# Performance work log

Hardware: AMD Instinct MI355X
Metric: run time of the kernel (lower is better)

Reference implementation:

```python
import jax, jax.numpy as jnp
import numpy as np

EMB_DIM = 400
NUM_ENT = 100000
NUM_REL = 200
OUT_CH = 6
STRIDE = 2
MAX_ARITY = 3
ARITY = 3
BATCH = 8192
W_OUT = (EMB_DIM - 1) // STRIDE + 1          # conv output width (filt_w=1, stride=2)
FC_LEN = OUT_CH * W_OUT                      # 1200


def setup_inputs() -> dict:
    key = jax.random.key(0)
    ks = jax.random.split(key, 10)
    r_idx = jax.random.randint(ks[0], (BATCH,), 0, NUM_REL)
    E_mat = jax.random.randint(ks[1], (BATCH, ARITY), 0, NUM_ENT)
    ms = jax.random.normal(ks[2], (BATCH, ARITY), dtype=jnp.float32)
    bs = jax.random.normal(ks[3], (BATCH, ARITY), dtype=jnp.float32)
    E_emb = jax.random.normal(ks[4], (NUM_ENT, EMB_DIM), dtype=jnp.float32) * 0.05
    R_emb = jax.random.normal(ks[5], (NUM_REL, EMB_DIM), dtype=jnp.float32) * 0.05
    fc2_W = jax.random.normal(ks[6], (OUT_CH, MAX_ARITY + 1), dtype=jnp.float32) * 0.1
    fc2_b = jax.random.normal(ks[7], (OUT_CH,), dtype=jnp.float32) * 0.1
    fc_W = jax.random.normal(ks[8], (EMB_DIM, FC_LEN), dtype=jnp.float32) * 0.02
    fc_b = jax.random.normal(ks[9], (EMB_DIM,), dtype=jnp.float32) * 0.02
    return {"r_idx": r_idx, "E_mat": E_mat, "ms": ms, "bs": bs,
            "E_emb": E_emb, "R_emb": R_emb,
            "fc2_W": fc2_W, "fc2_b": fc2_b, "fc_W": fc_W, "fc_b": fc_b}


def _convolve(E_emb, fc2_W, fc2_b, fc_W, fc_b, e_idx, pos):
    # Embedding gather: (B, D)
    e = E_emb[e_idx]
    # 1x1 grouped conv with stride=2 == strided slice of the embedding: (B, W_OUT)
    e_s = e[:, ::STRIDE]
    # Hypernetwork filter from fc2(one_hot(pos)) -- identical across batch: (OUT_CH,)
    k = fc2_W[:, pos] + fc2_b
    # Per-sample outer product, flattened oc-major (matches torch view order): (B, FC_LEN)
    feat = (k[None, :, None] * e_s[:, None, :]).reshape(e.shape[0], FC_LEN)
    # fc: Linear(FC_LEN, EMB_DIM)
    return jnp.einsum('bf,df->bd', feat, fc_W) + fc_b


def reference(r_idx, E_mat, ms, bs, E_emb, R_emb, fc2_W, fc2_b, fc_W, fc_b):
    r = R_emb[r_idx]                                        # (B, D)
    x = None
    for i in range(E_mat.shape[1]):                         # small fixed arity loop
        e = _convolve(E_emb, fc2_W, fc2_b, fc_W, fc_b, E_mat[:, i], i)
        e = e * ms[:, i][:, None] + bs[:, i][:, None]
        x = e if x is None else x * e
    x = x * r
    return jnp.sum(x, axis=1)                               # (B,)
```

## Files before the change

### kernel.cpp

```cpp
#include <hip/hip_runtime.h>

typedef __attribute__((ext_vector_type(8))) short bf16x8;
typedef __attribute__((ext_vector_type(4))) float f32x4;

#define EMB_DIM 400
#define OUT_CH  6
#define ARITY   3
#define BATCH   8192
#define W_OUT   200
#define FC_LEN  1200
#define NT      25
#define NKS     7
#define BM      32
#define NTASK   (ARITY * BM * 100)
#define NLD     19

static __device__ __forceinline__ ushort f2bf(float f) {
    union { float f; uint u; } v; v.f = f;
    uint u = v.u;
    return (ushort)((u + 0x7FFF + ((u >> 16) & 1)) >> 16);
}

__global__ __launch_bounds__(256)
void pack_M(const float* __restrict__ fc2_W, const float* __restrict__ fc2_b,
            const float* __restrict__ fc_W, ushort* __restrict__ Mb) {
    __shared__ float Bt[32][16];
    const int bid = blockIdx.x;
    const int kk  = blockIdx.y;
    const int i = bid / NT, t = bid % NT;
    float kc[OUT_CH];
#pragma unroll
    for (int c = 0; c < OUT_CH; ++c) kc[c] = fc2_W[c * 4 + i] + fc2_b[c];
    const int tid = threadIdx.x;
    const int dd = tid >> 4, wl = tid & 15;
    const int d = t * 16 + dd;
#pragma unroll
    for (int s = 0; s < 2; ++s) {
        int w = kk * 32 + wl + 16 * s;
        float v = 0.f;
        if (w < W_OUT) {
#pragma unroll
            for (int c = 0; c < OUT_CH; ++c)
                v = fmaf(kc[c], fc_W[d * FC_LEN + c * W_OUT + w], v);
        }
        Bt[wl + 16 * s][dd] = v;
    }
    __syncthreads();
    if (tid < 64) {
        const int l = tid;
        ushort vals[8];
#pragma unroll
        for (int j = 0; j < 8; ++j)
            vals[j] = f2bf(Bt[(l >> 4) * 8 + j][l & 15]);
        *reinterpret_cast<uint4*>(Mb + ((size_t)(bid * NKS + kk) * 64 + l) * 8) =
            *reinterpret_cast<const uint4*>(vals);
    }
}

__global__ __launch_bounds__(512)
void hype_mfma(const int* __restrict__ r_idx, const int* __restrict__ E_mat,
               const float* __restrict__ ms, const float* __restrict__ bs,
               const float* __restrict__ E_emb, const float* __restrict__ R_emb,
               const float* __restrict__ fc_b, const ushort* __restrict__ Mb,
               float* __restrict__ out) {
    __shared__ ushort es[ARITY * 2 * NKS * 64 * 8];
    __shared__ float sm_ms[BM * 3], sm_bs[BM * 3], sm_fcb[EMB_DIM];
    __shared__ int   sm_rb[BM], sm_ent[BM * 3];
    __shared__ float osum[4][BM];

    const int tid = threadIdx.x;
    const int b0 = blockIdx.x * BM;

    if (tid < BM * 3) {
        sm_ms[tid]  = ms[b0 * 3 + tid];
        sm_bs[tid]  = bs[b0 * 3 + tid];
        sm_ent[tid] = E_mat[b0 * 3 + tid];
    }
    if (tid >= 96 && tid < 96 + BM) sm_rb[tid - 96] = r_idx[b0 + tid - 96] * EMB_DIM;
    for (int z = tid; z < EMB_DIM; z += 512) sm_fcb[z] = fc_b[z];

    uint* esu = reinterpret_cast<uint*>(es);
    for (int z = tid; z < ARITY * 2 * 192; z += 512) {
        int pair = z / 192, off = z % 192;
        esu[(pair * NKS + 6) * 256 + 64 + off] = 0;
    }
    __syncthreads();

    float4 vreg[NLD];
#pragma unroll
    for (int k = 0; k < NLD; ++k) {
        int tq = tid + k * 512;
        if (tq < NTASK) {
            int q = tq % 100;
            int p = tq / 100;
            int i = p / BM, r = p % BM;
            int ent = sm_ent[r * 3 + i];
            vreg[k] = *reinterpret_cast<const float4*>(
                E_emb + (size_t)ent * EMB_DIM + 4 * q);
        }
    }
#pragma unroll
    for (int k = 0; k < NLD; ++k) {
        int tq = tid + k * 512;
        if (tq < NTASK) {
            int q = tq % 100;
            int p = tq / 100;
            int i = p / BM, r = p % BM;
            int w = 2 * q;
            int kk = w >> 5;
            int lsub = (w >> 3) & 3;
            int j = w & 7;
            int rg = r >> 4, rl = r & 15;
            int l = lsub * 16 + rl;
            uint pk = (uint)f2bf(vreg[k].x) | ((uint)f2bf(vreg[k].z) << 16);
            esu[(((i * 2 + rg) * NKS + kk) * 64 + l) * 4 + (j >> 1)] = pk;
        }
    }
    __syncthreads();

    const int wid = tid >> 6;
    const int lane = tid & 63;
    const int rg = wid & 1, cg = wid >> 1;
    const int cl = lane & 15;
    const int rql = lane >> 4;

    bf16x8 afrag[ARITY][NKS];
#pragma unroll
    for (int i = 0; i < ARITY; ++i)
#pragma unroll
        for (int kk = 0; kk < NKS; ++kk)
            afrag[i][kk] = *reinterpret_cast<const bf16x8*>(
                es + (((i * 2 + rg) * NKS + kk) * 64 + lane) * 8);

    float msv[ARITY][4], bsv[ARITY][4];
    int rbv[4];
#pragma unroll
    for (int r_ = 0; r_ < 4; ++r_) {
        int row = rg * 16 + rql * 4 + r_;
#pragma unroll
        for (int i = 0; i < ARITY; ++i) {
            msv[i][r_] = sm_ms[row * 3 + i];
            bsv[i][r_] = sm_bs[row * 3 + i];
        }
        rbv[r_] = sm_rb[row];
    }

    float rowsum[4] = {0.f, 0.f, 0.f, 0.f};
    for (int t = cg; t < NT; t += 4) {
        f32x4 acc[ARITY];
#pragma unroll
        for (int i = 0; i < ARITY; ++i) {
            f32x4 a = {0.f, 0.f, 0.f, 0.f};
            const ushort* bp = Mb + ((size_t)(i * NT + t) * NKS * 64 + lane) * 8;
#pragma unroll
            for (int kk = 0; kk < NKS; ++kk) {
                bf16x8 bfr = *reinterpret_cast<const bf16x8*>(bp + kk * 512);
                a = __builtin_amdgcn_mfma_f32_16x16x32_bf16(afrag[i][kk], bfr, a, 0, 0, 0);
            }
            acc[i] = a;
        }
        const int d = t * 16 + cl;
        const float fcb = sm_fcb[d];
#pragma unroll
        for (int r_ = 0; r_ < 4; ++r_) {
            float Rr = R_emb[rbv[r_] + d];
            float e0 = fmaf(acc[0][r_] + fcb, msv[0][r_], bsv[0][r_]);
            float e1 = fmaf(acc[1][r_] + fcb, msv[1][r_], bsv[1][r_]);
            float e2 = fmaf(acc[2][r_] + fcb, msv[2][r_], bsv[2][r_]);
            rowsum[r_] = fmaf(e0 * e1 * e2, Rr, rowsum[r_]);
        }
    }

#pragma unroll
    for (int m = 1; m < 16; m <<= 1)
#pragma unroll
        for (int r_ = 0; r_ < 4; ++r_)
            rowsum[r_] += __shfl_xor(rowsum[r_], m, 64);
    if (cl == 0) {
#pragma unroll
        for (int r_ = 0; r_ < 4; ++r_)
            osum[cg][rg * 16 + rql * 4 + r_] = rowsum[r_];
    }
    __syncthreads();
    if (tid < BM)
        out[b0 + tid] = osum[0][tid] + osum[1][tid] + osum[2][tid] + osum[3][tid];
}

extern "C" void kernel_launch(void* const* d_in, const int* in_sizes, int n_in,
                              void* d_out, int out_size, void* d_ws, size_t ws_size,
                              hipStream_t stream) {
    const int*   r_idx = (const int*)d_in[0];
    const int*   E_mat = (const int*)d_in[1];
    const float* ms    = (const float*)d_in[2];
    const float* bs    = (const float*)d_in[3];
    const float* E_emb = (const float*)d_in[4];
    const float* R_emb = (const float*)d_in[5];
    const float* fc2_W = (const float*)d_in[6];
    const float* fc2_b = (const float*)d_in[7];
    const float* fc_W  = (const float*)d_in[8];
    const float* fc_b  = (const float*)d_in[9];
    float*  out = (float*)d_out;
    ushort* Mb  = (ushort*)d_ws;

    pack_M<<<dim3(ARITY * NT, NKS), 256, 0, stream>>>(fc2_W, fc2_b, fc_W, Mb);
    hype_mfma<<<BATCH / BM, 512, 0, stream>>>(r_idx, E_mat, ms, bs, E_emb, R_emb,
                                              fc_b, Mb, out);
}
```

Measured before the change: 34.08 us.

## Have each wave cover both row groups to reuse B fragments across MFMAs

Each wave now loads A fragments for both 16-row groups and computes both against the same B fragment, with column tiles split across 8 waves instead of 4. This halves global loads of the packed weight matrix per block and doubles MFMA work per B load. It raises register pressure, since the A fragments double, and gives coarser load balance over the 25 column tiles. The per-row scale, bias and index values are now read from shared memory inside the loop instead of being held in registers.

After: 44.77 us. +31.4%, slower.

```diff
diff --git a/kernel.cpp b/kernel.cpp
--- a/kernel.cpp
+++ b/kernel.cpp
@@ -66,7 +66,7 @@
     __shared__ ushort es[ARITY * 2 * NKS * 64 * 8];
     __shared__ float sm_ms[BM * 3], sm_bs[BM * 3], sm_fcb[EMB_DIM];
     __shared__ int   sm_rb[BM], sm_ent[BM * 3];
-    __shared__ float osum[4][BM];
+    __shared__ float osum[8][BM];
 
     const int tid = threadIdx.x;
     const int b0 = blockIdx.x * BM;
@@ -118,72 +118,76 @@
     }
     __syncthreads();
 
-    const int wid = tid >> 6;
+    const int wv   = tid >> 6;
     const int lane = tid & 63;
-    const int rg = wid & 1, cg = wid >> 1;
-    const int cl = lane & 15;
-    const int rql = lane >> 4;
-
-    bf16x8 afrag[ARITY][NKS];
-#pragma unroll
-    for (int i = 0; i < ARITY; ++i)
-#pragma unroll
-        for (int kk = 0; kk < NKS; ++kk)
-            afrag[i][kk] = *reinterpret_cast<const bf16x8*>(
-                es + (((i * 2 + rg) * NKS + kk) * 64 + lane) * 8);
-
-    float msv[ARITY][4], bsv[ARITY][4];
-    int rbv[4];
-#pragma unroll
-    for (int r_ = 0; r_ < 4; ++r_) {
-        int row = rg * 16 + rql * 4 + r_;
+    const int cl   = lane & 15;
+    const int rql  = lane >> 4;
+
+    bf16x8 afrag[2][ARITY][NKS];
+#pragma unroll
+    for (int rg = 0; rg < 2; ++rg)
+#pragma unroll
+        for (int i = 0; i < ARITY; ++i)
+#pragma unroll
+            for (int kk = 0; kk < NKS; ++kk)
+                afrag[rg][i][kk] = *reinterpret_cast<const bf16x8*>(
+                    es + (((i * 2 + rg) * NKS + kk) * 64 + lane) * 8);
+
+    float rowsum[2][4] = {{0.f, 0.f, 0.f, 0.f}, {0.f, 0.f, 0.f, 0.f}};
+    for (int t = wv; t < NT; t += 8) {
+        f32x4 acc[2][ARITY];
+#pragma unroll
+        for (int rg = 0; rg < 2; ++rg)
+#pragma unroll
+            for (int i = 0; i < ARITY; ++i) acc[rg][i] = (f32x4){0.f, 0.f, 0.f, 0.f};
 #pragma unroll
         for (int i = 0; i < ARITY; ++i) {
-            msv[i][r_] = sm_ms[row * 3 + i];
-            bsv[i][r_] = sm_bs[row * 3 + i];
-        }
-        rbv[r_] = sm_rb[row];
-    }
-
-    float rowsum[4] = {0.f, 0.f, 0.f, 0.f};
-    for (int t = cg; t < NT; t += 4) {
-        f32x4 acc[ARITY];
-#pragma unroll
-        for (int i = 0; i < ARITY; ++i) {
-            f32x4 a = {0.f, 0.f, 0.f, 0.f};
             const ushort* bp = Mb + ((size_t)(i * NT + t) * NKS * 64 + lane) * 8;
 #pragma unroll
             for (int kk = 0; kk < NKS; ++kk) {
                 bf16x8 bfr = *reinterpret_cast<const bf16x8*>(bp + kk * 512);
-                a = __builtin_amdgcn_mfma_f32_16x16x32_bf16(afrag[i][kk], bfr, a, 0, 0, 0);
+                acc[0][i] = __builtin_amdgcn_mfma_f32_16x16x32_bf16(
+                    afrag[0][i][kk], bfr, acc[0][i], 0, 0, 0);
+                acc[1][i] = __builtin_amdgcn_mfma_f32_16x16x32_bf16(
+                    afrag[1][i][kk], bfr, acc[1][i], 0, 0, 0);
             }
-            acc[i] = a;
         }
         const int d = t * 16 + cl;
         const float fcb = sm_fcb[d];
 #pragma unroll
-        for (int r_ = 0; r_ < 4; ++r_) {
-            float Rr = R_emb[rbv[r_] + d];
-            float e0 = fmaf(acc[0][r_] + fcb, msv[0][r_], bsv[0][r_]);
-            float e1 = fmaf(acc[1][r_] + fcb, msv[1][r_], bsv[1][r_]);
-            float e2 = fmaf(acc[2][r_] + fcb, msv[2][r_], bsv[2][r_]);
-            rowsum[r_] = fmaf(e0 * e1 * e2, Rr, rowsum[r_]);
-        }
+        for (int rg = 0; rg < 2; ++rg)
+#pragma unroll
+            for (int r_ = 0; r_ < 4; ++r_) {
+                int row = rg * 16 + rql * 4 + r_;
+                float Rr = R_emb[sm_rb[row] + d];
+                float e0 = fmaf(acc[rg][0][r_] + fcb, sm_ms[row * 3 + 0], sm_bs[row * 3 + 0]);
+                float e1 = fmaf(acc[rg][1][r_] + fcb, sm_ms[row * 3 + 1], sm_bs[row * 3 + 1]);
+                float e2 = fmaf(acc[rg][2][r_] + fcb, sm_ms[row * 3 + 2], sm_bs[row * 3 + 2]);
+                rowsum[rg][r_] = fmaf(e0 * e1 * e2, Rr, rowsum[rg][r_]);
+            }
     }
 
 #pragma unroll
     for (int m = 1; m < 16; m <<= 1)
 #pragma unroll
-        for (int r_ = 0; r_ < 4; ++r_)
-            rowsum[r_] += __shfl_xor(rowsum[r_], m, 64);
+        for (int rg = 0; rg < 2; ++rg)
+#pragma unroll
+            for (int r_ = 0; r_ < 4; ++r_)
+                rowsum[rg][r_] += __shfl_xor(rowsum[rg][r_], m, 64);
     if (cl == 0) {
 #pragma unroll
-        for (int r_ = 0; r_ < 4; ++r_)
-            osum[cg][rg * 16 + rql * 4 + r_] = rowsum[r_];
-    }
-    __syncthreads();
-    if (tid < BM)
-        out[b0 + tid] = osum[0][tid] + osum[1][tid] + osum[2][tid] + osum[3][tid];
+        for (int rg = 0; rg < 2; ++rg)
+#pragma unroll
+            for (int r_ = 0; r_ < 4; ++r_)
+                osum[wv][rg * 16 + rql * 4 + r_] = rowsum[rg][r_];
+    }
+    __syncthreads();
+    if (tid < BM) {
+        float s = 0.f;
+#pragma unroll
+        for (int w = 0; w < 8; ++w) s += osum[w][tid];
+        out[b0 + tid] = s;
+    }
 }
 
 extern "C" void kernel_launch(void* const* d_in, const int* in_sizes, int n_in,
```

## Fuse weight packing into main kernel with grid-wide atomic barrier

Applied to the files above, without the earlier changes.

Merges the pack_M kernel into the main MFMA kernel: each of the 256 blocks packs a share of the bf16 weight slices, then signals completion through a global atomic counter. Blocks overlap their embedding gather and LDS staging with the packing phase, and spin on the counter before the MFMA loop. This removes one kernel launch and the serialization gap between the two kernels, at the cost of a memset, a spin barrier that relies on all 256 blocks being co-resident, and packing work now sitting on the critical path inside each block. It also hoists the R_emb loads ahead of the MFMA chain.

New measurement: 71.81 us. +110.7%, slower.

```diff
diff --git a/kernel.cpp b/kernel.cpp
--- a/kernel.cpp
+++ b/kernel.cpp
@@ -12,6 +12,8 @@
 #define NT      25
 #define NKS     7
 #define BM      32
+#define NBLK    256
+#define NSLICE  (ARITY * NT * NKS)
 #define NTASK   (ARITY * BM * 100)
 #define NLD     19
 
@@ -21,49 +23,16 @@
     return (ushort)((u + 0x7FFF + ((u >> 16) & 1)) >> 16);
 }
 
-__global__ __launch_bounds__(256)
-void pack_M(const float* __restrict__ fc2_W, const float* __restrict__ fc2_b,
-            const float* __restrict__ fc_W, ushort* __restrict__ Mb) {
+__global__ __launch_bounds__(512)
+void hype_fused(const int* __restrict__ r_idx, const int* __restrict__ E_mat,
+                const float* __restrict__ ms, const float* __restrict__ bs,
+                const float* __restrict__ E_emb, const float* __restrict__ R_emb,
+                const float* __restrict__ fc2_W, const float* __restrict__ fc2_b,
+                const float* __restrict__ fc_W, const float* __restrict__ fc_b,
+                ushort* __restrict__ Mb, uint* __restrict__ done,
+                float* __restrict__ out) {
+    __shared__ ushort es[ARITY * 2 * NKS * 64 * 8];
     __shared__ float Bt[32][16];
-    const int bid = blockIdx.x;
-    const int kk  = blockIdx.y;
-    const int i = bid / NT, t = bid % NT;
-    float kc[OUT_CH];
-#pragma unroll
-    for (int c = 0; c < OUT_CH; ++c) kc[c] = fc2_W[c * 4 + i] + fc2_b[c];
-    const int tid = threadIdx.x;
-    const int dd = tid >> 4, wl = tid & 15;
-    const int d = t * 16 + dd;
-#pragma unroll
-    for (int s = 0; s < 2; ++s) {
-        int w = kk * 32 + wl + 16 * s;
-        float v = 0.f;
-        if (w < W_OUT) {
-#pragma unroll
-            for (int c = 0; c < OUT_CH; ++c)
-                v = fmaf(kc[c], fc_W[d * FC_LEN + c * W_OUT + w], v);
-        }
-        Bt[wl + 16 * s][dd] = v;
-    }
-    __syncthreads();
-    if (tid < 64) {
-        const int l = tid;
-        ushort vals[8];
-#pragma unroll
-        for (int j = 0; j < 8; ++j)
-            vals[j] = f2bf(Bt[(l >> 4) * 8 + j][l & 15]);
-        *reinterpret_cast<uint4*>(Mb + ((size_t)(bid * NKS + kk) * 64 + l) * 8) =
-            *reinterpret_cast<const uint4*>(vals);
-    }
-}
-
-__global__ __launch_bounds__(512)
-void hype_mfma(const int* __restrict__ r_idx, const int* __restrict__ E_mat,
-               const float* __restrict__ ms, const float* __restrict__ bs,
-               const float* __restrict__ E_emb, const float* __restrict__ R_emb,
-               const float* __restrict__ fc_b, const ushort* __restrict__ Mb,
-               float* __restrict__ out) {
-    __shared__ ushort es[ARITY * 2 * NKS * 64 * 8];
     __shared__ float sm_ms[BM * 3], sm_bs[BM * 3], sm_fcb[EMB_DIM];
     __shared__ int   sm_rb[BM], sm_ent[BM * 3];
     __shared__ float osum[4][BM];
@@ -84,7 +53,42 @@
         int pair = z / 192, off = z % 192;
         esu[(pair * NKS + 6) * 256 + 64 + off] = 0;
     }
-    __syncthreads();
+
+    for (int s = blockIdx.x; s < NSLICE; s += NBLK) {
+        const int bt = s / NKS, kk = s % NKS;
+        const int i = bt / NT, t = bt % NT;
+        if (tid < 256) {
+            float kc[OUT_CH];
+#pragma unroll
+            for (int c = 0; c < OUT_CH; ++c) kc[c] = fc2_W[c * 4 + i] + fc2_b[c];
+            const int dd = tid >> 4, wl = tid & 15;
+            const int d = t * 16 + dd;
+#pragma unroll
+            for (int ss = 0; ss < 2; ++ss) {
+                int w = kk * 32 + wl + 16 * ss;
+                float v = 0.f;
+                if (w < W_OUT) {
+#pragma unroll
+                    for (int c = 0; c < OUT_CH; ++c)
+                        v = fmaf(kc[c], fc_W[d * FC_LEN + c * W_OUT + w], v);
+                }
+                Bt[wl + 16 * ss][dd] = v;
+            }
+        }
+        __syncthreads();
+        if (tid < 64) {
+            const int l = tid;
+            ushort vals[8];
+#pragma unroll
+            for (int j = 0; j < 8; ++j)
+                vals[j] = f2bf(Bt[(l >> 4) * 8 + j][l & 15]);
+            *reinterpret_cast<uint4*>(Mb + ((size_t)(bt * NKS + kk) * 64 + l) * 8) =
+                *reinterpret_cast<const uint4*>(vals);
+        }
+        __syncthreads();
+    }
+    __threadfence();
+    if (tid == 0) atomicAdd(done, 1u);
 
     float4 vreg[NLD];
 #pragma unroll
@@ -145,8 +149,22 @@
         rbv[r_] = sm_rb[row];
     }
 
+    if (tid == 0) {
+        while (__hip_atomic_load(done, __ATOMIC_ACQUIRE, __HIP_MEMORY_SCOPE_AGENT)
+               < (uint)NBLK) {
+            __builtin_amdgcn_s_sleep(8);
+        }
+    }
+    __syncthreads();
+
     float rowsum[4] = {0.f, 0.f, 0.f, 0.f};
     for (int t = cg; t < NT; t += 4) {
+        const int d = t * 16 + cl;
+        float Rr[4];
+#pragma unroll
+        for (int r_ = 0; r_ < 4; ++r_) Rr[r_] = R_emb[rbv[r_] + d];
+        const float fcb = sm_fcb[d];
+
         f32x4 acc[ARITY];
 #pragma unroll
         for (int i = 0; i < ARITY; ++i) {
@@ -159,15 +177,12 @@
             }
             acc[i] = a;
         }
-        const int d = t * 16 + cl;
-        const float fcb = sm_fcb[d];
 #pragma unroll
         for (int r_ = 0; r_ < 4; ++r_) {
-            float Rr = R_emb[rbv[r_] + d];
             float e0 = fmaf(acc[0][r_] + fcb, msv[0][r_], bsv[0][r_]);
             float e1 = fmaf(acc[1][r_] + fcb, msv[1][r_], bsv[1][r_]);
             float e2 = fmaf(acc[2][r_] + fcb, msv[2][r_], bsv[2][r_]);
-            rowsum[r_] = fmaf(e0 * e1 * e2, Rr, rowsum[r_]);
+            rowsum[r_] = fmaf(e0 * e1 * e2, Rr[r_], rowsum[r_]);
         }
     }
 
@@ -199,10 +214,11 @@
     const float* fc2_b = (const float*)d_in[7];
     const float* fc_W  = (const float*)d_in[8];
     const float* fc_b  = (const float*)d_in[9];
-    float*  out = (float*)d_out;
-    ushort* Mb  = (ushort*)d_ws;
-
-    pack_M<<<dim3(ARITY * NT, NKS), 256, 0, stream>>>(fc2_W, fc2_b, fc_W, Mb);
-    hype_mfma<<<BATCH / BM, 512, 0, stream>>>(r_idx, E_mat, ms, bs, E_emb, R_emb,
-                                              fc_b, Mb, out);
+    float*  out  = (float*)d_out;
+    ushort* Mb   = (ushort*)d_ws;
+    uint*   done = (uint*)((char*)d_ws + 537600);
+
+    hipMemsetAsync(done, 0, sizeof(uint), stream);
+    hype_fused<<<NBLK, 512, 0, stream>>>(r_idx, E_mat, ms, bs, E_emb, R_emb,
+                                         fc2_W, fc2_b, fc_W, fc_b, Mb, done, out);
 }
```

## Move embedding gather into prep kernel alongside weight packing, GEMM reads pre-packed A

Applied to the files above, without the earlier changes.

The embedding gather and bf16 packing of A fragments move out of the GEMM kernel into the first kernel. That kernel now runs the M-packing blocks and the gather blocks side by side in one grid, so the gather no longer waits behind pack_M and no longer sits on the GEMM's critical path. The GEMM kernel reads pre-packed A fragments straight from global workspace and drops its LDS staging and syncs. The cost is an extra global round-trip of about 16 MB of bf16 A data through the workspace. The workspace size must also hold the new Af region.

Result: slower. 38.59 us (+13.2%).

```diff
diff --git a/kernel.cpp b/kernel.cpp
--- a/kernel.cpp
+++ b/kernel.cpp
@@ -12,8 +12,12 @@
 #define NT      25
 #define NKS     7
 #define BM      32
+#define NSLICE  (ARITY * NT * NKS)
+#define PACK_BLKS 263
+#define GATHER_BLKS (BATCH / BM)
 #define NTASK   (ARITY * BM * 100)
 #define NLD     19
+#define AF_U16_PER_BLK (ARITY * 2 * NKS * 64 * 8)
 
 static __device__ __forceinline__ ushort f2bf(float f) {
     union { float f; uint u; } v; v.f = f;
@@ -21,128 +25,127 @@
     return (ushort)((u + 0x7FFF + ((u >> 16) & 1)) >> 16);
 }
 
-__global__ __launch_bounds__(256)
-void pack_M(const float* __restrict__ fc2_W, const float* __restrict__ fc2_b,
-            const float* __restrict__ fc_W, ushort* __restrict__ Mb) {
-    __shared__ float Bt[32][16];
-    const int bid = blockIdx.x;
-    const int kk  = blockIdx.y;
-    const int i = bid / NT, t = bid % NT;
-    float kc[OUT_CH];
-#pragma unroll
-    for (int c = 0; c < OUT_CH; ++c) kc[c] = fc2_W[c * 4 + i] + fc2_b[c];
+__global__ __launch_bounds__(512)
+void prep2(const int* __restrict__ E_mat, const float* __restrict__ E_emb,
+           const float* __restrict__ fc2_W, const float* __restrict__ fc2_b,
+           const float* __restrict__ fc_W,
+           ushort* __restrict__ Mb, ushort* __restrict__ Af) {
+    __shared__ float Bt[2][32][16];
+    __shared__ int   sm_ent[BM * 3];
     const int tid = threadIdx.x;
-    const int dd = tid >> 4, wl = tid & 15;
-    const int d = t * 16 + dd;
-#pragma unroll
-    for (int s = 0; s < 2; ++s) {
-        int w = kk * 32 + wl + 16 * s;
-        float v = 0.f;
-        if (w < W_OUT) {
-#pragma unroll
-            for (int c = 0; c < OUT_CH; ++c)
-                v = fmaf(kc[c], fc_W[d * FC_LEN + c * W_OUT + w], v);
-        }
-        Bt[wl + 16 * s][dd] = v;
-    }
-    __syncthreads();
-    if (tid < 64) {
-        const int l = tid;
-        ushort vals[8];
-#pragma unroll
-        for (int j = 0; j < 8; ++j)
-            vals[j] = f2bf(Bt[(l >> 4) * 8 + j][l & 15]);
-        *reinterpret_cast<uint4*>(Mb + ((size_t)(bid * NKS + kk) * 64 + l) * 8) =
-            *reinterpret_cast<const uint4*>(vals);
+
+    if (blockIdx.x < PACK_BLKS) {
+        const int half = tid >> 8, htid = tid & 255;
+        const int s = blockIdx.x * 2 + half;
+        const bool valid = s < NSLICE;
+        int i = 0, t = 0, kk = 0, bt = 0;
+        if (valid) { bt = s / NKS; kk = s % NKS; i = bt / NT; t = bt % NT; }
+        if (valid) {
+            float kc[OUT_CH];
+#pragma unroll
+            for (int c = 0; c < OUT_CH; ++c) kc[c] = fc2_W[c * 4 + i] + fc2_b[c];
+            const int dd = htid >> 4, wl = htid & 15;
+            const int d = t * 16 + dd;
+#pragma unroll
+            for (int ss = 0; ss < 2; ++ss) {
+                int w = kk * 32 + wl + 16 * ss;
+                float v = 0.f;
+                if (w < W_OUT) {
+#pragma unroll
+                    for (int c = 0; c < OUT_CH; ++c)
+                        v = fmaf(kc[c], fc_W[d * FC_LEN + c * W_OUT + w], v);
+                }
+                Bt[half][wl + 16 * ss][dd] = v;
+            }
+        }
+        __syncthreads();
+        if (valid && htid < 64) {
+            const int l = htid;
+            ushort vals[8];
+#pragma unroll
+            for (int j = 0; j < 8; ++j)
+                vals[j] = f2bf(Bt[half][(l >> 4) * 8 + j][l & 15]);
+            *reinterpret_cast<uint4*>(Mb + ((size_t)(bt * NKS + kk) * 64 + l) * 8) =
+                *reinterpret_cast<const uint4*>(vals);
+        }
+    } else {
+        const int g = blockIdx.x - PACK_BLKS;
+        const int b0 = g * BM;
+        if (tid < BM * 3) sm_ent[tid] = E_mat[b0 * 3 + tid];
+        uint* Afu = reinterpret_cast<uint*>(Af) + (size_t)g * (AF_U16_PER_BLK / 2);
+        for (int z = tid; z < ARITY * 2 * 192; z += 512) {
+            int pair = z / 192, off = z % 192;
+            Afu[(pair * NKS + 6) * 256 + 64 + off] = 0;
+        }
+        __syncthreads();
+
+        float4 vreg[NLD];
+#pragma unroll
+        for (int k = 0; k < NLD; ++k) {
+            int tq = tid + k * 512;
+            if (tq < NTASK) {
+                int q = tq % 100;
+                int p = tq / 100;
+                int i = p / BM, r = p % BM;
+                int ent = sm_ent[r * 3 + i];
+                vreg[k] = *reinterpret_cast<const float4*>(
+                    E_emb + (size_t)ent * EMB_DIM + 4 * q);
+            }
+        }
+#pragma unroll
+        for (int k = 0; k < NLD; ++k) {
+            int tq = tid + k * 512;
+            if (tq < NTASK) {
+                int q = tq % 100;
+                int p = tq / 100;
+                int i = p / BM, r = p % BM;
+                int w = 2 * q;
+                int kk = w >> 5;
+                int lsub = (w >> 3) & 3;
+                int j = w & 7;
+                int rg = r >> 4, rl = r & 15;
+                int l = lsub * 16 + rl;
+                uint pk = (uint)f2bf(vreg[k].x) | ((uint)f2bf(vreg[k].z) << 16);
+                Afu[(((i * 2 + rg) * NKS + kk) * 64 + l) * 4 + (j >> 1)] = pk;
+            }
+        }
     }
 }
 
 __global__ __launch_bounds__(512)
-void hype_mfma(const int* __restrict__ r_idx, const int* __restrict__ E_mat,
-               const float* __restrict__ ms, const float* __restrict__ bs,
-               const float* __restrict__ E_emb, const float* __restrict__ R_emb,
-               const float* __restrict__ fc_b, const ushort* __restrict__ Mb,
-               float* __restrict__ out) {
-    __shared__ ushort es[ARITY * 2 * NKS * 64 * 8];
-    __shared__ float sm_ms[BM * 3], sm_bs[BM * 3], sm_fcb[EMB_DIM];
-    __shared__ int   sm_rb[BM], sm_ent[BM * 3];
+void gemm2(const int* __restrict__ r_idx, const float* __restrict__ ms,
+           const float* __restrict__ bs, const float* __restrict__ R_emb,
+           const float* __restrict__ fc_b, const ushort* __restrict__ Mb,
+           const ushort* __restrict__ Af, float* __restrict__ out) {
     __shared__ float osum[4][BM];
-
     const int tid = threadIdx.x;
     const int b0 = blockIdx.x * BM;
-
-    if (tid < BM * 3) {
-        sm_ms[tid]  = ms[b0 * 3 + tid];
-        sm_bs[tid]  = bs[b0 * 3 + tid];
-        sm_ent[tid] = E_mat[b0 * 3 + tid];
-    }
-    if (tid >= 96 && tid < 96 + BM) sm_rb[tid - 96] = r_idx[b0 + tid - 96] * EMB_DIM;
-    for (int z = tid; z < EMB_DIM; z += 512) sm_fcb[z] = fc_b[z];
-
-    uint* esu = reinterpret_cast<uint*>(es);
-    for (int z = tid; z < ARITY * 2 * 192; z += 512) {
-        int pair = z / 192, off = z % 192;
-        esu[(pair * NKS + 6) * 256 + 64 + off] = 0;
-    }
-    __syncthreads();
-
-    float4 vreg[NLD];
-#pragma unroll
-    for (int k = 0; k < NLD; ++k) {
-        int tq = tid + k * 512;
-        if (tq < NTASK) {
-            int q = tq % 100;
-            int p = tq / 100;
-            int i = p / BM, r = p % BM;
-            int ent = sm_ent[r * 3 + i];
-            vreg[k] = *reinterpret_cast<const float4*>(
-                E_emb + (size_t)ent * EMB_DIM + 4 * q);
-        }
-    }
-#pragma unroll
-    for (int k = 0; k < NLD; ++k) {
-        int tq = tid + k * 512;
-        if (tq < NTASK) {
-            int q = tq % 100;
-            int p = tq / 100;
-            int i = p / BM, r = p % BM;
-            int w = 2 * q;
-            int kk = w >> 5;
-            int lsub = (w >> 3) & 3;
-            int j = w & 7;
-            int rg = r >> 4, rl = r & 15;
-            int l = lsub * 16 + rl;
-            uint pk = (uint)f2bf(vreg[k].x) | ((uint)f2bf(vreg[k].z) << 16);
-            esu[(((i * 2 + rg) * NKS + kk) * 64 + l) * 4 + (j >> 1)] = pk;
-        }
-    }
-    __syncthreads();
-
     const int wid = tid >> 6;
     const int lane = tid & 63;
     const int rg = wid & 1, cg = wid >> 1;
     const int cl = lane & 15;
     const int rql = lane >> 4;
 
+    const ushort* Ab = Af + (size_t)blockIdx.x * AF_U16_PER_BLK;
     bf16x8 afrag[ARITY][NKS];
 #pragma unroll
     for (int i = 0; i < ARITY; ++i)
 #pragma unroll
         for (int kk = 0; kk < NKS; ++kk)
             afrag[i][kk] = *reinterpret_cast<const bf16x8*>(
-                es + (((i * 2 + rg) * NKS + kk) * 64 + lane) * 8);
+                Ab + (((i * 2 + rg) * NKS + kk) * 64 + lane) * 8);
 
     float msv[ARITY][4], bsv[ARITY][4];
     int rbv[4];
 #pragma unroll
     for (int r_ = 0; r_ < 4; ++r_) {
-        int row = rg * 16 + rql * 4 + r_;
+        int b = b0 + rg * 16 + rql * 4 + r_;
 #pragma unroll
         for (int i = 0; i < ARITY; ++i) {
-            msv[i][r_] = sm_ms[row * 3 + i];
-            bsv[i][r_] = sm_bs[row * 3 + i];
-        }
-        rbv[r_] = sm_rb[row];
+            msv[i][r_] = ms[b * 3 + i];
+            bsv[i][r_] = bs[b * 3 + i];
+        }
+        rbv[r_] = r_idx[b] * EMB_DIM;
     }
 
     float rowsum[4] = {0.f, 0.f, 0.f, 0.f};
@@ -160,7 +163,7 @@
             acc[i] = a;
         }
         const int d = t * 16 + cl;
-        const float fcb = sm_fcb[d];
+        const float fcb = fc_b[d];
 #pragma unroll
         for (int r_ = 0; r_ < 4; ++r_) {
             float Rr = R_emb[rbv[r_] + d];
@@ -201,8 +204,9 @@
     const float* fc_b  = (const float*)d_in[9];
     float*  out = (float*)d_out;
     ushort* Mb  = (ushort*)d_ws;
-
-    pack_M<<<dim3(ARITY * NT, NKS), 256, 0, stream>>>(fc2_W, fc2_b, fc_W, Mb);
-    hype_mfma<<<BATCH / BM, 512, 0, stream>>>(r_idx, E_mat, ms, bs, E_emb, R_emb,
-                                              fc_b, Mb, out);
-}
+    ushort* Af  = (ushort*)((char*)d_ws + 537600);
+
+    prep2<<<PACK_BLKS + GATHER_BLKS, 512, 0, stream>>>(E_mat, E_emb, fc2_W, fc2_b,
+                                                       fc_W, Mb, Af);
+    gemm2<<<GATHER_BLKS, 512, 0, stream>>>(r_idx, ms, bs, R_emb, fc_b, Mb, Af, out);
+}
```
